# Performance work log

Hardware: AMD Instinct MI355X
Metric: run time of the kernel (lower is better)

Reference implementation:

```python
import jax, jax.numpy as jnp
import numpy as np

H = 12        # num_attention_heads
A = 16        # agent_num
C = 768       # hidden_size


def setup_inputs() -> dict:
    key = jax.random.key(0)
    ks = jax.random.split(key, 16)
    B, N = 8, 4096
    std = 0.02
    return {
        "s1_hidden_states": jax.random.normal(ks[0], (B, N, C), jnp.float32),
        "s2_hidden_states": jax.random.normal(ks[1], (B, N, C), jnp.float32),
        "Wq": jax.random.normal(ks[2], (C, C), jnp.float32) * std,
        "bq": jnp.zeros((C,), jnp.float32),
        "Wk": jax.random.normal(ks[3], (C, C), jnp.float32) * std,
        "bk": jnp.zeros((C,), jnp.float32),
        "Wv": jax.random.normal(ks[4], (C, C), jnp.float32) * std,
        "bv": jnp.zeros((C,), jnp.float32),
        "an_bias": jax.random.normal(ks[5], (H, A, 7, 7), jnp.float32) * std,
        "na_bias": jax.random.normal(ks[6], (H, A, 7, 7), jnp.float32) * std,
        "ah_bias": jax.random.normal(ks[7], (1, H, A, A, 1), jnp.float32) * std,
        "aw_bias": jax.random.normal(ks[8], (1, H, A, 1, A), jnp.float32) * std,
        "ha_bias": jax.random.normal(ks[9], (1, H, A, 1, A), jnp.float32) * std,
        "wa_bias": jax.random.normal(ks[10], (1, H, 1, A, A), jnp.float32) * std,
    }


def reference(s1_hidden_states, s2_hidden_states, Wq, bq, Wk, bk, Wv, bv,
              an_bias, na_bias, ah_bias, aw_bias, ha_bias, wa_bias):
    b, n, c = s1_hidden_states.shape
    m = s2_hidden_states.shape[1]
    hd = c // H
    scale = hd ** -0.5

    q = s1_hidden_states @ Wq.T + bq            # (b, n, c)
    k = s2_hidden_states @ Wk.T + bk            # (b, m, c)
    v = s2_hidden_states @ Wv.T + bv            # (b, m, c)

    # AdaptiveAvgPool1d(A) with n % A == 0 -> uniform chunk mean
    agent = q.reshape(b, A, n // A, c).mean(axis=2)  # (b, A, c)

    def heads(x):
        return x.reshape(b, -1, H, hd).transpose(0, 2, 1, 3)

    qh, kh, vh = heads(q), heads(k), heads(v)        # (b,H,·,hd)
    ah = heads(agent)                                # (b,H,A,hd)

    # stage 1: agent -> keys.  bias is constant per (h, a) row.
    pb1 = jax.image.resize(an_bias, (H, A, A, A), method='bilinear').reshape(1, H, A, A * A)
    pb2 = (ah_bias + aw_bias).reshape(1, H, A, A * A)
    pb = (pb1 + pb2).mean(axis=-1)                   # (1, H, A)
    agent_attn = jnp.einsum('bhad,bhmd->bham', ah * scale, kh) + pb[:, :, :, None]
    agent_attn = jax.nn.softmax(agent_attn, axis=-1)
    agent_v = jnp.einsum('bham,bhmd->bhad', agent_attn, vh)  # (b,H,A,hd)

    # stage 2: queries -> agents.
    ab1 = jax.image.resize(na_bias, (H, A, A, A), method='bilinear') \
            .reshape(1, H, A, A * A).transpose(0, 1, 3, 2)   # (1,H,A*A,A)
    ab2 = (ha_bias + wa_bias).reshape(1, H, A * A, A)
    ab = (ab1 + ab2).mean(axis=-2)                   # (1, H, A)
    q_attn = jnp.einsum('bhnd,bhad->bhna', qh * scale, ah) + ab[:, :, None, :]
    q_attn = jax.nn.softmax(q_attn, axis=-1)
    x = jnp.einsum('bhna,bhad->bhnd', q_attn, agent_v)  # (b,H,n,hd)
    return x.transpose(0, 2, 1, 3).reshape(b, n, c)
```

## Files before the change

kernel.cpp:

```cpp
#include <hip/hip_runtime.h>
#include <cstdint>
#include <cstddef>

typedef unsigned short ushort_t;
typedef unsigned int uint;

typedef __attribute__((ext_vector_type(8))) short short8;
typedef __attribute__((ext_vector_type(4))) float floatx4;

#define CDIM 768

__device__ __forceinline__ float bfu(ushort_t u) {
    return __uint_as_float(((uint)u) << 16);
}
__device__ __forceinline__ void bf2(uint u, float& lo, float& hi) {
    lo = __uint_as_float(u << 16);
    hi = __uint_as_float(u & 0xffff0000u);
}
__device__ __forceinline__ ushort_t f2bfu(float f) {
    uint u = __float_as_uint(f);
    u += 0x7fffu + ((u >> 16) & 1u);
    return (ushort_t)(u >> 16);
}
__device__ __forceinline__ uint pack2(float a, float b) {
    return (uint)f2bfu(a) | ((uint)f2bfu(b) << 16);
}
__device__ __forceinline__ uint cvt2(float lo, float hi) {
    uint r;
    asm("v_cvt_pk_bf16_f32 %0, %1, %2" : "=v"(r) : "v"(lo), "v"(hi));
    return r;
}
__device__ __forceinline__ short8 mk8(uint a, uint b, uint c, uint d) {
    union { uint4 u; short8 s; } x;
    x.u = (uint4){a, b, c, d};
    return x.s;
}
__device__ __forceinline__ void gload_lds16(const void* g, void* l) {
    __builtin_amdgcn_global_load_lds(
        (__attribute__((address_space(1))) void*)(uintptr_t)g,
        (__attribute__((address_space(3))) void*)l, 16, 0, 0);
}

__global__ __launch_bounds__(256) void cvt_w(
    const float* __restrict__ Wq, const float* __restrict__ Wk,
    const float* __restrict__ Wv, ushort_t* __restrict__ wb)
{
    const int m = blockIdx.y;
    const float* src = (m == 0) ? Wq : (m == 1 ? Wk : Wv);
    ushort_t* dst = wb + (size_t)m * 589824;
    const int i = (blockIdx.x * 256 + threadIdx.x) * 8;
    const float4 f0 = *(const float4*)(src + i);
    const float4 f1 = *(const float4*)(src + i + 4);
    uint4 u;
    u.x = pack2(f0.x, f0.y);
    u.y = pack2(f0.z, f0.w);
    u.z = pack2(f1.x, f1.y);
    u.w = pack2(f1.z, f1.w);
    *(uint4*)(dst + i) = u;
}

__global__ __launch_bounds__(256) void cvt_a(
    const float* __restrict__ s1, const float* __restrict__ s2,
    ushort_t* __restrict__ ab)
{
    const int m = blockIdx.y;
    const float* src = (m == 0) ? s1 : s2;
    ushort_t* dst = ab + (size_t)m * 25165824;
    const size_t i = ((size_t)blockIdx.x * 256 + threadIdx.x) * 8;
    const float4 f0 = *(const float4*)(src + i);
    const float4 f1 = *(const float4*)(src + i + 4);
    uint4 u;
    u.x = pack2(f0.x, f0.y);
    u.y = pack2(f0.z, f0.w);
    u.z = pack2(f1.x, f1.y);
    u.w = pack2(f1.z, f1.w);
    *(uint4*)(dst + i) = u;
}

__global__ __launch_bounds__(256) void init_agent(const float* __restrict__ bq,
                                                  float* __restrict__ agent)
{
    const int bh = blockIdx.x;
    const int h = bh % 12;
    for (int i = threadIdx.x; i < 1024; i += 256)
        agent[(size_t)bh * 1024 + i] = bq[h * 64 + (i & 63)];
}

__global__ __launch_bounds__(256, 2) void gemm_qkv(
    const ushort_t* __restrict__ ab, const ushort_t* __restrict__ wb,
    const float* __restrict__ bq, const float* __restrict__ bk, const float* __restrict__ bv,
    ushort_t* __restrict__ qo, ushort_t* __restrict__ ko, ushort_t* __restrict__ vo,
    float* __restrict__ agent)
{
    const int z = blockIdx.z;
    const ushort_t* A     = ab + (size_t)(z != 0) * 25165824;
    const ushort_t* W     = wb + (size_t)z * 589824;
    const float* bias     = (z == 0) ? bq : (z == 1 ? bk : bv);
    ushort_t* out         = (z == 0) ? qo : (z == 1 ? ko : vo);

    __shared__ ushort_t At[128 * 64];
    __shared__ ushort_t Wt[128 * 64];

    const int tid  = threadIdx.x;
    const int wave = tid >> 6;
    const int lane = tid & 63;
    const int wm = wave >> 1, wn = wave & 1;

    const int id   = blockIdx.x + (blockIdx.y << 8);
    const int id2  = (id & 7) * 192 + (id >> 3);
    const int row0 = (id2 / 6) * 128;
    const int col0 = (id2 % 6) * 128;

    const int sro = lane >> 3;
    const int sch = ((lane & 7) ^ sro) * 8;
    const ushort_t* gaBase = A + (size_t)(row0 + wave * 32 + sro) * CDIM + sch;
    const ushort_t* gwBase = W + (size_t)(col0 + wave * 32 + sro) * CDIM + sch;

    floatx4 acc[4][4];
    #pragma unroll
    for (int i = 0; i < 4; ++i)
        #pragma unroll
        for (int j = 0; j < 4; ++j)
            acc[i][j] = (floatx4){0.f, 0.f, 0.f, 0.f};

    const int q4 = lane >> 4, r16 = lane & 15;

    for (int kt = 0; kt < CDIM; kt += 64) {
        __syncthreads();
        #pragma unroll
        for (int i = 0; i < 4; ++i) {
            gload_lds16(gaBase + (size_t)i * 8 * CDIM + kt, &At[(wave * 32 + i * 8) * 64]);
            gload_lds16(gwBase + (size_t)i * 8 * CDIM + kt, &Wt[(wave * 32 + i * 8) * 64]);
        }
        __syncthreads();
        #pragma unroll
        for (int ks = 0; ks < 2; ++ks) {
            short8 af[4], bfr[4];
            #pragma unroll
            for (int mt = 0; mt < 4; ++mt) {
                const int row = wm * 64 + mt * 16 + r16;
                const int ch  = (ks * 4 + q4) ^ (row & 7);
                af[mt] = *(const short8*)&At[row * 64 + ch * 8];
            }
            #pragma unroll
            for (int nt = 0; nt < 4; ++nt) {
                const int row = wn * 64 + nt * 16 + r16;
                const int ch  = (ks * 4 + q4) ^ (row & 7);
                bfr[nt] = *(const short8*)&Wt[row * 64 + ch * 8];
            }
            #pragma unroll
            for (int mt = 0; mt < 4; ++mt)
                #pragma unroll
                for (int nt = 0; nt < 4; ++nt)
                    acc[mt][nt] = __builtin_amdgcn_mfma_f32_16x16x32_bf16(
                        af[mt], bfr[nt], acc[mt][nt], 0, 0, 0);
        }
    }

    const int b = row0 >> 12;
    const int m_base = row0 & 4095;
    #pragma unroll
    for (int nt = 0; nt < 4; ++nt) {
        const int col = col0 + wn * 64 + nt * 16 + r16;
        const int h = col >> 6, d = col & 63;
        const float bb = bias[col];
        ushort_t* ob = out + ((size_t)(b * 12 + h) * 4096) * 64 + d;
        float psum = 0.f;
        #pragma unroll
        for (int mt = 0; mt < 4; ++mt) {
            const int m = m_base + wm * 64 + mt * 16 + q4 * 4;
            #pragma unroll
            for (int r = 0; r < 4; ++r) {
                ob[(size_t)(m + r) * 64] = f2bfu(acc[mt][nt][r] + bb);
                psum += acc[mt][nt][r];
            }
        }
        if (z == 0) {
            psum += __shfl_xor(psum, 16);
            psum += __shfl_xor(psum, 32);
            if (q4 == 0)
                atomicAdd(&agent[(size_t)(b * 12 + h) * 1024 + (m_base >> 8) * 64 + d],
                          psum * (1.0f / 256.0f));
        }
    }
}

__global__ void bias_ab_k(const float* __restrict__ na, const float* __restrict__ ha,
                          const float* __restrict__ wa, float* __restrict__ ab)
{
    const int t = threadIdx.x;
    if (t >= 192) return;
    const int h = t >> 4, a = t & 15;
    const float cw[7] = {2.25f, 2.34375f, 2.28125f, 2.25f, 2.28125f, 2.34375f, 2.25f};
    float acc = 0.f;
    const float* nb = na + (h * 16 + a) * 49;
    for (int i = 0; i < 7; ++i)
        for (int j = 0; j < 7; ++j)
            acc += cw[i] * cw[j] * nb[i * 7 + j];
    acc *= (1.0f / 256.0f);
    float s = 0.f;
    for (int p = 0; p < 16; ++p)
        s += ha[(h * 16 + p) * 16 + a] + wa[(h * 16 + p) * 16 + a];
    ab[t] = acc + s * (1.0f / 16.0f);
}

__global__ __launch_bounds__(512) void stage1(
    const ushort_t* __restrict__ k_hm, const ushort_t* __restrict__ v_hm,
    const float* __restrict__ agent, float* __restrict__ Sp, float* __restrict__ avp)
{
    const int bh = blockIdx.x, z = blockIdx.y;
    const int tid = threadIdx.x;
    __shared__ float ahs[1024];
    __shared__ ushort_t E2[512 * 20];

    for (int i = tid; i < 1024; i += 512)
        ahs[i] = agent[(size_t)bh * 1024 + i] * 0.125f;
    __syncthreads();

    const int m0 = z * 512;
    const ushort_t* kb = k_hm + ((size_t)bh * 4096 + m0) * 64;

    {
        const uint4* kr = (const uint4*)(kb + (size_t)tid * 64);
        uint ku[16];
        #pragma unroll
        for (int i = 0; i < 4; ++i) {
            uint4 ua = kr[i];
            ku[i*4+0] = ua.x; ku[i*4+1] = ua.y; ku[i*4+2] = ua.z; ku[i*4+3] = ua.w;
        }
        float ds[16];
        #pragma unroll
        for (int a = 0; a < 16; ++a) ds[a] = 0.f;
        #pragma unroll
        for (int c = 0; c < 16; ++c) {
            float a0, a1, a2, a3;
            bf2(ku[2*c],   a0, a1); bf2(ku[2*c+1], a2, a3);
            #pragma unroll
            for (int a = 0; a < 16; ++a) {
                const floatx4 av = *(const floatx4*)&ahs[a * 64 + c * 4];
                ds[a] += a0 * av[0] + a1 * av[1] + a2 * av[2] + a3 * av[3];
            }
        }
        uint e[8];
        #pragma unroll
        for (int a2 = 0; a2 < 8; ++a2)
            e[a2] = pack2(__expf(ds[2*a2]), __expf(ds[2*a2+1]));
        uint2* dA = (uint2*)&E2[(size_t)tid * 20];
        dA[0] = make_uint2(e[0], e[1]); dA[1] = make_uint2(e[2], e[3]);
        dA[2] = make_uint2(e[4], e[5]); dA[3] = make_uint2(e[6], e[7]);
    }
    __syncthreads();

    const int d = tid & 63, g = (tid >> 6) & 3, half = tid >> 8;
    const int mb = half * 256;
    const ushort_t* vb = v_hm + ((size_t)bh * 4096 + m0 + mb) * 64 + d;
    float acc0 = 0, acc1 = 0, acc2 = 0, acc3 = 0;
    float ss0 = 0, ss1 = 0, ss2 = 0, ss3 = 0;
    for (int ml = 0; ml < 256; ++ml) {
        const float vv = bfu(vb[(size_t)ml * 64]);
        const uint2 ee = *(const uint2*)&E2[(size_t)(mb + ml) * 20 + g * 4];
        float e0, e1, e2, e3;
        bf2(ee.x, e0, e1);
        bf2(ee.y, e2, e3);
        acc0 += e0 * vv; ss0 += e0;
        acc1 += e1 * vv; ss1 += e1;
        acc2 += e2 * vv; ss2 += e2;
        acc3 += e3 * vv; ss3 += e3;
    }
    const int z2 = z * 2 + half;
    float* avz = avp + (size_t)(z2 * 96 + bh) * 1024;
    avz[(g * 4 + 0) * 64 + d] = acc0;
    avz[(g * 4 + 1) * 64 + d] = acc1;
    avz[(g * 4 + 2) * 64 + d] = acc2;
    avz[(g * 4 + 3) * 64 + d] = acc3;
    if (d == 0) {
        float* Sz = Sp + (z2 * 96 + bh) * 16;
        Sz[g * 4 + 0] = ss0;
        Sz[g * 4 + 1] = ss1;
        Sz[g * 4 + 2] = ss2;
        Sz[g * 4 + 3] = ss3;
    }
}

__global__ __launch_bounds__(256) void stage2(
    const ushort_t* __restrict__ q_hm, const float* __restrict__ avp,
    const float* __restrict__ Sp, const float* __restrict__ agent,
    const float* __restrict__ ab, float* __restrict__ out)
{
    const int nb = blockIdx.x;
    const int bh = blockIdx.y;
    const int b = bh / 12, h = bh % 12;
    const int tid = threadIdx.x;
    const int g = (tid >> 4) & 3;
    const int t = tid & 15;
    const int w = tid >> 6;
    __shared__ float avn[1024];

    {
        const int i4 = tid * 4;
        const int a = i4 >> 6;
        floatx4 num = {0.f, 0.f, 0.f, 0.f};
        float den = 0.f;
        #pragma unroll
        for (int zz = 0; zz < 16; ++zz) {
            num += *(const floatx4*)&avp[(size_t)(zz * 96 + bh) * 1024 + i4];
            den += Sp[(zz * 96 + bh) * 16 + a];
        }
        const float r = 1.0f / den;
        *(floatx4*)&avn[i4] = num * r;
    }
    __syncthreads();

    short8 ahA[2], ahE[2];
    #pragma unroll
    for (int k0 = 0; k0 < 2; ++k0) {
        const float* p = agent + (size_t)bh * 1024 + t * 64 + k0 * 32 + g * 8;
        const float4 f0 = *(const float4*)p;
        const float4 f1 = *(const float4*)(p + 4);
        const float v[8] = {f0.x, f0.y, f0.z, f0.w, f1.x, f1.y, f1.z, f1.w};
        uint u[4], e[4];
        #pragma unroll
        for (int j = 0; j < 4; ++j) {
            const float a0 = v[2*j] * 0.125f, a1 = v[2*j+1] * 0.125f;
            u[j] = cvt2(a0, a1);
            float b0, b1; bf2(u[j], b0, b1);
            e[j] = cvt2(a0 - b0, a1 - b1);
        }
        ahA[k0] = mk8(u[0], u[1], u[2], u[3]);
        ahE[k0] = mk8(e[0], e[1], e[2], e[3]);
    }

    short8 avf[4], ave[4];
    #pragma unroll
    for (int dt = 0; dt < 4; ++dt) {
        uint u[4] = {0, 0, 0, 0}, e[4] = {0, 0, 0, 0};
        if (g < 2) {
            #pragma unroll
            for (int j = 0; j < 4; ++j) {
                const float a0 = avn[(8*g + 2*j)     * 64 + dt * 16 + t];
                const float a1 = avn[(8*g + 2*j + 1) * 64 + dt * 16 + t];
                u[j] = cvt2(a0, a1);
                float b0, b1; bf2(u[j], b0, b1);
                e[j] = cvt2(a0 - b0, a1 - b1);
            }
        }
        avf[dt] = mk8(u[0], u[1], u[2], u[3]);
        ave[dt] = mk8(e[0], e[1], e[2], e[3]);
    }

    float abv[4];
    #pragma unroll
    for (int r = 0; r < 4; ++r) abv[r] = ab[h * 16 + 4 * g + r];

    const int src0 = (t + 32 * g) & 63;
    const int src1 = (src0 + 16) & 63;
    const int n0 = nb * 256 + w * 64;
    const ushort_t* qb = q_hm + ((size_t)bh * 4096 + n0) * 64;
    float* ob = out + ((size_t)b * 4096 + n0) * CDIM + h * 64;

    #pragma unroll
    for (int ti = 0; ti < 4; ++ti) {
        const ushort_t* qp = qb + (size_t)(ti * 16 + t) * 64 + g * 8;
        const short8 qB0 = *(const short8*)(qp);
        const short8 qB1 = *(const short8*)(qp + 32);

        floatx4 sc = {0.f, 0.f, 0.f, 0.f};
        sc = __builtin_amdgcn_mfma_f32_16x16x32_bf16(ahA[0], qB0, sc, 0, 0, 0);
        sc = __builtin_amdgcn_mfma_f32_16x16x32_bf16(ahA[1], qB1, sc, 0, 0, 0);
        sc = __builtin_amdgcn_mfma_f32_16x16x32_bf16(ahE[0], qB0, sc, 0, 0, 0);
        sc = __builtin_amdgcn_mfma_f32_16x16x32_bf16(ahE[1], qB1, sc, 0, 0, 0);

        const float e0 = __expf(sc[0] + abv[0]);
        const float e1 = __expf(sc[1] + abv[1]);
        const float e2 = __expf(sc[2] + abv[2]);
        const float e3 = __expf(sc[3] + abv[3]);
        float s = e0 + e1 + e2 + e3;
        s += __shfl_xor(s, 16);
        s += __shfl_xor(s, 32);
        const float rs = 1.0f / s;
        const float p0 = e0 * rs, p1 = e1 * rs, p2 = e2 * rs, p3 = e3 * rs;

        const uint P0 = cvt2(p0, p1), P1 = cvt2(p2, p3);
        float q0, q1, q2, q3;
        bf2(P0, q0, q1); bf2(P1, q2, q3);
        const uint E0 = cvt2(p0 - q0, p1 - q1), E1 = cvt2(p2 - q2, p3 - q3);

        uint w0 = __shfl(P0, src0), w1 = __shfl(P1, src0);
        uint w2 = __shfl(P0, src1), w3 = __shfl(P1, src1);
        uint x0 = __shfl(E0, src0), x1 = __shfl(E1, src0);
        uint x2 = __shfl(E0, src1), x3 = __shfl(E1, src1);
        if (g >= 2) { w0 = w1 = w2 = w3 = 0; x0 = x1 = x2 = x3 = 0; }
        const short8 pf = mk8(w0, w1, w2, w3);
        const short8 pe = mk8(x0, x1, x2, x3);

        float* op = ob + (size_t)(ti * 16 + t) * CDIM + 4 * g;
        #pragma unroll
        for (int dt = 0; dt < 4; ++dt) {
            floatx4 od = {0.f, 0.f, 0.f, 0.f};
            od = __builtin_amdgcn_mfma_f32_16x16x32_bf16(avf[dt], pf, od, 0, 0, 0);
            od = __builtin_amdgcn_mfma_f32_16x16x32_bf16(avf[dt], pe, od, 0, 0, 0);
            od = __builtin_amdgcn_mfma_f32_16x16x32_bf16(ave[dt], pf, od, 0, 0, 0);
            *(floatx4*)(op + dt * 16) = od;
        }
    }
}

extern "C" void kernel_launch(void* const* d_in, const int* in_sizes, int n_in,
                              void* d_out, int out_size, void* d_ws, size_t ws_size,
                              hipStream_t stream) {
    (void)in_sizes; (void)n_in; (void)out_size; (void)ws_size;
    const float* s1 = (const float*)d_in[0];
    const float* s2 = (const float*)d_in[1];
    const float* Wq = (const float*)d_in[2];
    const float* bq = (const float*)d_in[3];
    const float* Wk = (const float*)d_in[4];
    const float* bk = (const float*)d_in[5];
    const float* Wv = (const float*)d_in[6];
    const float* bv = (const float*)d_in[7];
    const float* na = (const float*)d_in[9];
    const float* ha = (const float*)d_in[12];
    const float* wa = (const float*)d_in[13];
    float* out = (float*)d_out;

    char* ws = (char*)d_ws;
    ushort_t* q_hm = (ushort_t*)(ws);
    ushort_t* k_hm = (ushort_t*)(ws + 50331648);
    ushort_t* v_hm = (ushort_t*)(ws + 100663296);
    float* agent   = (float*)(ws + 150994944);
    float* Sp      = (float*)(ws + 151388160);
    float* ab      = (float*)(ws + 151486464);
    ushort_t* wb   = (ushort_t*)(ws + 151487232);
    ushort_t* abuf = (ushort_t*)(ws + 155026176);
    float* avp     = (float*)(ws + 155026176);

    cvt_w      <<<dim3(288, 3),    256, 0, stream>>>(Wq, Wk, Wv, wb);
    cvt_a      <<<dim3(12288, 2),  256, 0, stream>>>(s1, s2, abuf);
    init_agent <<<dim3(96),        256, 0, stream>>>(bq, agent);
    gemm_qkv   <<<dim3(256, 6, 3), 256, 0, stream>>>(abuf, wb, bq, bk, bv,
                                                     q_hm, k_hm, v_hm, agent);
    bias_ab_k  <<<1, 256, 0, stream>>>(na, ha, wa, ab);
    stage1     <<<dim3(96, 8),     512, 0, stream>>>(k_hm, v_hm, agent, Sp, avp);
    stage2     <<<dim3(16, 96),    256, 0, stream>>>(q_hm, avp, Sp, agent, ab, out);
}
```

Before: 312.5 us.

## Stage QKV GEMM epilogue through LDS for coalesced stores; merge small prep kernels

The GEMM epilogue now writes the biased bf16 tile into a padded shared-memory buffer and then copies it to the head-major Q/K/V outputs with 16-byte per-thread stores. Previously each lane issued scattered 2-byte stores, which is very inefficient for a write stream of this size. The weight conversion, agent init and bias-table kernels are merged into one `prep` launch to save launch overhead. In stage1, the key-row loads are hoisted into one batch of eight 16-byte loads. The cost is extra LDS traffic, two more barriers and more registers in the GEMM and stage1.

```diff
diff --git a/kernel.cpp b/kernel.cpp
--- a/kernel.cpp
+++ b/kernel.cpp
@@ -41,22 +41,48 @@
         (__attribute__((address_space(3))) void*)l, 16, 0, 0);
 }
 
-__global__ __launch_bounds__(256) void cvt_w(
+__global__ __launch_bounds__(256) void prep(
     const float* __restrict__ Wq, const float* __restrict__ Wk,
-    const float* __restrict__ Wv, ushort_t* __restrict__ wb)
+    const float* __restrict__ Wv, const float* __restrict__ bq,
+    const float* __restrict__ na, const float* __restrict__ ha,
+    const float* __restrict__ wa,
+    ushort_t* __restrict__ wb, float* __restrict__ agent, float* __restrict__ ab)
 {
-    const int m = blockIdx.y;
-    const float* src = (m == 0) ? Wq : (m == 1 ? Wk : Wv);
-    ushort_t* dst = wb + (size_t)m * 589824;
-    const int i = (blockIdx.x * 256 + threadIdx.x) * 8;
-    const float4 f0 = *(const float4*)(src + i);
-    const float4 f1 = *(const float4*)(src + i + 4);
-    uint4 u;
-    u.x = pack2(f0.x, f0.y);
-    u.y = pack2(f0.z, f0.w);
-    u.z = pack2(f1.x, f1.y);
-    u.w = pack2(f1.z, f1.w);
-    *(uint4*)(dst + i) = u;
+    const int bid = blockIdx.x;
+    if (bid < 864) {
+        const int m = bid / 288;
+        const float* src = (m == 0) ? Wq : (m == 1 ? Wk : Wv);
+        ushort_t* dst = wb + (size_t)m * 589824;
+        const int i = ((bid % 288) * 256 + threadIdx.x) * 8;
+        const float4 f0 = *(const float4*)(src + i);
+        const float4 f1 = *(const float4*)(src + i + 4);
+        uint4 u;
+        u.x = pack2(f0.x, f0.y);
+        u.y = pack2(f0.z, f0.w);
+        u.z = pack2(f1.x, f1.y);
+        u.w = pack2(f1.z, f1.w);
+        *(uint4*)(dst + i) = u;
+    } else if (bid < 960) {
+        const int bh = bid - 864;
+        const int h = bh % 12;
+        for (int i = threadIdx.x; i < 1024; i += 256)
+            agent[(size_t)bh * 1024 + i] = bq[h * 64 + (i & 63)];
+    } else {
+        const int t = threadIdx.x;
+        if (t >= 192) return;
+        const int h = t >> 4, a = t & 15;
+        const float cw[7] = {2.25f, 2.34375f, 2.28125f, 2.25f, 2.28125f, 2.34375f, 2.25f};
+        float acc = 0.f;
+        const float* nb = na + (h * 16 + a) * 49;
+        for (int i = 0; i < 7; ++i)
+            for (int j = 0; j < 7; ++j)
+                acc += cw[i] * cw[j] * nb[i * 7 + j];
+        acc *= (1.0f / 256.0f);
+        float s = 0.f;
+        for (int p = 0; p < 16; ++p)
+            s += ha[(h * 16 + p) * 16 + a] + wa[(h * 16 + p) * 16 + a];
+        ab[t] = acc + s * (1.0f / 16.0f);
+    }
 }
 
 __global__ __launch_bounds__(256) void cvt_a(
@@ -77,15 +103,6 @@
     *(uint4*)(dst + i) = u;
 }
 
-__global__ __launch_bounds__(256) void init_agent(const float* __restrict__ bq,
-                                                  float* __restrict__ agent)
-{
-    const int bh = blockIdx.x;
-    const int h = bh % 12;
-    for (int i = threadIdx.x; i < 1024; i += 256)
-        agent[(size_t)bh * 1024 + i] = bq[h * 64 + (i & 63)];
-}
-
 __global__ __launch_bounds__(256, 2) void gemm_qkv(
     const ushort_t* __restrict__ ab, const ushort_t* __restrict__ wb,
     const float* __restrict__ bq, const float* __restrict__ bk, const float* __restrict__ bv,
@@ -98,8 +115,9 @@
     const float* bias     = (z == 0) ? bq : (z == 1 ? bk : bv);
     ushort_t* out         = (z == 0) ? qo : (z == 1 ? ko : vo);
 
-    __shared__ ushort_t At[128 * 64];
-    __shared__ ushort_t Wt[128 * 64];
+    __shared__ ushort_t lds[17408];
+    ushort_t* At = lds;
+    ushort_t* Wt = lds + 8192;
 
     const int tid  = threadIdx.x;
     const int wave = tid >> 6;
@@ -157,51 +175,45 @@
         }
     }
 
+    __syncthreads();
     const int b = row0 >> 12;
     const int m_base = row0 & 4095;
     #pragma unroll
     for (int nt = 0; nt < 4; ++nt) {
-        const int col = col0 + wn * 64 + nt * 16 + r16;
-        const int h = col >> 6, d = col & 63;
-        const float bb = bias[col];
-        ushort_t* ob = out + ((size_t)(b * 12 + h) * 4096) * 64 + d;
+        const int coll = wn * 64 + nt * 16 + r16;
+        const float bb = bias[col0 + coll];
         float psum = 0.f;
         #pragma unroll
         for (int mt = 0; mt < 4; ++mt) {
-            const int m = m_base + wm * 64 + mt * 16 + q4 * 4;
+            const int rowl = wm * 64 + mt * 16 + q4 * 4;
             #pragma unroll
             for (int r = 0; r < 4; ++r) {
-                ob[(size_t)(m + r) * 64] = f2bfu(acc[mt][nt][r] + bb);
+                lds[(rowl + r) * 136 + coll] = f2bfu(acc[mt][nt][r] + bb);
                 psum += acc[mt][nt][r];
             }
         }
         if (z == 0) {
             psum += __shfl_xor(psum, 16);
             psum += __shfl_xor(psum, 32);
-            if (q4 == 0)
+            if (q4 == 0) {
+                const int h = (col0 + coll) >> 6, d = (col0 + coll) & 63;
                 atomicAdd(&agent[(size_t)(b * 12 + h) * 1024 + (m_base >> 8) * 64 + d],
                           psum * (1.0f / 256.0f));
-        }
-    }
-}
-
-__global__ void bias_ab_k(const float* __restrict__ na, const float* __restrict__ ha,
-                          const float* __restrict__ wa, float* __restrict__ ab)
-{
-    const int t = threadIdx.x;
-    if (t >= 192) return;
-    const int h = t >> 4, a = t & 15;
-    const float cw[7] = {2.25f, 2.34375f, 2.28125f, 2.25f, 2.28125f, 2.34375f, 2.25f};
-    float acc = 0.f;
-    const float* nb = na + (h * 16 + a) * 49;
-    for (int i = 0; i < 7; ++i)
-        for (int j = 0; j < 7; ++j)
-            acc += cw[i] * cw[j] * nb[i * 7 + j];
-    acc *= (1.0f / 256.0f);
-    float s = 0.f;
-    for (int p = 0; p < 16; ++p)
-        s += ha[(h * 16 + p) * 16 + a] + wa[(h * 16 + p) * 16 + a];
-    ab[t] = acc + s * (1.0f / 16.0f);
+            }
+        }
+    }
+    __syncthreads();
+    #pragma unroll
+    for (int it = 0; it < 8; ++it) {
+        const int task  = it * 256 + tid;
+        const int chunk = task & 7;
+        const int rh    = task >> 3;
+        const int rowl  = rh >> 1, hl = rh & 1;
+        const uint4 v = *(const uint4*)&lds[rowl * 136 + hl * 64 + chunk * 8];
+        ushort_t* op = out + ((size_t)(b * 12 + (col0 >> 6) + hl) * 4096
+                              + m_base + rowl) * 64 + chunk * 8;
+        *(uint4*)op = v;
+    }
 }
 
 __global__ __launch_bounds__(512) void stage1(
@@ -222,9 +234,9 @@
 
     {
         const uint4* kr = (const uint4*)(kb + (size_t)tid * 64);
-        uint ku[16];
-        #pragma unroll
-        for (int i = 0; i < 4; ++i) {
+        uint ku[32];
+        #pragma unroll
+        for (int i = 0; i < 8; ++i) {
             uint4 ua = kr[i];
             ku[i*4+0] = ua.x; ku[i*4+1] = ua.y; ku[i*4+2] = ua.z; ku[i*4+3] = ua.w;
         }
@@ -433,12 +445,11 @@
     ushort_t* abuf = (ushort_t*)(ws + 155026176);
     float* avp     = (float*)(ws + 155026176);
 
-    cvt_w      <<<dim3(288, 3),    256, 0, stream>>>(Wq, Wk, Wv, wb);
-    cvt_a      <<<dim3(12288, 2),  256, 0, stream>>>(s1, s2, abuf);
-    init_agent <<<dim3(96),        256, 0, stream>>>(bq, agent);
-    gemm_qkv   <<<dim3(256, 6, 3), 256, 0, stream>>>(abuf, wb, bq, bk, bv,
-                                                     q_hm, k_hm, v_hm, agent);
-    bias_ab_k  <<<1, 256, 0, stream>>>(na, ha, wa, ab);
-    stage1     <<<dim3(96, 8),     512, 0, stream>>>(k_hm, v_hm, agent, Sp, avp);
-    stage2     <<<dim3(16, 96),    256, 0, stream>>>(q_hm, avp, Sp, agent, ab, out);
-}
+    prep     <<<dim3(961),       256, 0, stream>>>(Wq, Wk, Wv, bq, na, ha, wa,
+                                                   wb, agent, ab);
+    cvt_a    <<<dim3(12288, 2),  256, 0, stream>>>(s1, s2, abuf);
+    gemm_qkv <<<dim3(256, 6, 3), 256, 0, stream>>>(abuf, wb, bq, bk, bv,
+                                                   q_hm, k_hm, v_hm, agent);
+    stage1   <<<dim3(96, 8),     512, 0, stream>>>(k_hm, v_hm, agent, Sp, avp);
+    stage2   <<<dim3(16, 96),    256, 0, stream>>>(q_hm, avp, Sp, agent, ab, out);
+}
```

New measurement: 295.8 us. -5.3%, faster.
